# Optimization experiments

Measured on AMD Instinct MI355X. Metric: run time of the kernel, lower is better.

## Reference

```python
import jax, jax.numpy as jnp
import numpy as np

DV = 512   # node feature size
DE = 256   # edge feature size
N = 128    # valid node num (human_nums + obj_nums)
B = 8
K = 3      # propagate_layers
C = 117    # hoi_classes


def gru_cell(x, h, w_ih, w_hh, b_ih, b_hh):
    # PyTorch nn.GRU single step, gate order (r, z, n)
    gi = w_ih @ x + b_ih
    gh = w_hh @ h + b_hh
    ir, iz, inn = jnp.split(gi, 3)
    hr, hz, hn = jnp.split(gh, 3)
    r = jax.nn.sigmoid(ir + hr)
    z = jax.nn.sigmoid(iz + hz)
    n = jnp.tanh(inn + r * hn)
    return (1.0 - z) * n + z * h


def _run_graph(h, e, w_link, b_link, w_msg, b_msg, w_ih, w_hh, b_ih, b_hh):
    # h: [dv, N], e: [de, N, N]
    wl_j = w_link[:DV]          # applied to Feature[:dv, i, :] = h (column index j)
    wl_i = w_link[DV:2 * DV]    # applied to Feature[dv:2dv, :, i] = h (row index i)
    wl_e = w_link[2 * DV:]
    adj = jnp.zeros((N, N), h.dtype)
    for _ in range(K):
        # link function on Feature built under torch.no_grad -> stop_gradient
        hs = jax.lax.stop_gradient(h)
        es = jax.lax.stop_gradient(e)
        logits = (wl_i @ hs)[:, None] + (wl_j @ hs)[None, :] \
                 + jnp.einsum('c,cij->ij', wl_e, es) + b_link
        adj = jax.nn.sigmoid(logits)  # [N, N]

        def node_step(carry, i):
            h, e = carry
            h_v = h[:, i]                      # [dv]
            e_row = e[:, i, :]                 # [de, N] (rows < i already updated this round)
            comb = jnp.concatenate(
                [jnp.broadcast_to(h_v[:, None], (DV, N)), h, e_row], axis=0)  # [2dv+de, N]
            m = jax.nn.relu(w_msg @ comb + b_msg[:, None])                    # [de, N]
            e = e.at[:, i, :].set(m)
            m_sum = (m * adj[i][None, :]).sum(axis=1)                         # [de]
            h_new = gru_cell(m_sum, h_v, w_ih, w_hh, b_ih, b_hh)
            h = h.at[:, i].set(h_new)
            return (h, e), None

        (h, e), _ = jax.lax.scan(node_step, (h, e), jnp.arange(N))
    return adj, h


def setup_inputs() -> dict:
    key = jax.random.key(0)
    ks = jax.random.split(key, 8)
    s = 0.02
    return {
        "edge_features": jax.random.normal(ks[0], (B, N, N, DE), jnp.float32),
        "node_features": jax.random.normal(ks[1], (B, N, DV), jnp.float32),
        "adj_mat": jnp.zeros((B, N, N), jnp.float32),
        "node_labels": jnp.zeros((B, N, C), jnp.float32),
        "human_nums": jnp.full((B,), 32, jnp.int32),
        "obj_nums": jnp.full((B,), 96, jnp.int32),
        "w_link": jax.random.normal(ks[2], (2 * DV + DE,), jnp.float32) * s,
        "b_link": jnp.zeros((), jnp.float32),
        "w_msg": jax.random.normal(ks[3], (DE, 2 * DV + DE), jnp.float32) * s,
        "b_msg": jnp.zeros((DE,), jnp.float32),
        "w_ih": jax.random.normal(ks[4], (3 * DV, DE), jnp.float32) * s,
        "w_hh": jax.random.normal(ks[5], (3 * DV, DV), jnp.float32) * s,
        "b_ih": jnp.zeros((3 * DV,), jnp.float32),
        "b_hh": jnp.zeros((3 * DV,), jnp.float32),
        "w_ro": jax.random.normal(ks[6], (C, DV), jnp.float32) * s,
        "b_ro": jnp.zeros((C,), jnp.float32),
    }


def reference(edge_features, node_features, adj_mat, node_labels, human_nums,
              obj_nums, w_link, b_link, w_msg, b_msg, w_ih, w_hh, b_ih, b_hh,
              w_ro, b_ro):
    e0 = jnp.transpose(edge_features, (0, 3, 1, 2))  # [B, de, N, N]
    h0 = jnp.transpose(node_features, (0, 2, 1))     # [B, dv, N]
    run = jax.vmap(_run_graph, in_axes=(0, 0) + (None,) * 8)
    pred_adj_mat, h = run(h0, e0, w_link, b_link, w_msg, b_msg,
                          w_ih, w_hh, b_ih, b_hh)
    # readout on the final (post-last-update) node states
    pred_node_labels = jnp.einsum('cd,bdn->bnc', w_ro, h) + b_ro
    return pred_adj_mat, pred_node_labels
```

## Files before the change

### kernel.cpp

```cpp
#include <hip/hip_runtime.h>
#include <math.h>


#define NB 8
#define NN 128
#define DVV 512
#define DEE 256
#define NCC 117
#define SB 16
#define PGOFF 196608

typedef __attribute__((ext_vector_type(8))) short short8;
typedef __attribute__((ext_vector_type(4))) float f32x4;

__device__ __forceinline__ float sigmf(float x) {
  x = fminf(fmaxf(x, -30.f), 30.f);
  return 1.0f / (1.0f + __expf(-x));
}
__device__ __forceinline__ float tanhf_fast(float x) {
  x = fminf(fmaxf(x, -15.f), 15.f);
  float e = __expf(2.0f * x);
  return (e - 1.0f) / (e + 1.0f);
}
__device__ __forceinline__ unsigned short f2bf(float f) {
  union { float f; unsigned u; } v; v.f = f;
  unsigned u = v.u + 0x7FFFu + ((v.u >> 16) & 1u);
  return (unsigned short)(u >> 16);
}
__device__ __forceinline__ float bfu(unsigned short u) {
  union { unsigned u; float f; } v; v.u = ((unsigned)u) << 16; return v.f;
}

__global__ __launch_bounds__(256) void k_copy(const float* __restrict__ src, float* __restrict__ dst,
                                              unsigned short* __restrict__ hb) {
  int i = blockIdx.x * 256 + threadIdx.x;
  float4 v = ((const float4*)src)[i];
  ((float4*)dst)[i] = v;
  unsigned long long pk = (unsigned long long)f2bf(v.x) | ((unsigned long long)f2bf(v.y) << 16)
                        | ((unsigned long long)f2bf(v.z) << 32) | ((unsigned long long)f2bf(v.w) << 48);
  *(unsigned long long*)&hb[i * 4] = pk;
}

__global__ __launch_bounds__(256) void k_cvtw(const float* __restrict__ w_msg,
                                              unsigned short* __restrict__ w3b) {
  int idx = blockIdx.x * 256 + threadIdx.x;
  int r = idx >> 8, c = idx & 255;
  w3b[idx] = f2bf(w_msg[(size_t)r * 1280 + 1024 + c]);
}

__global__ __launch_bounds__(128) void k_av(const float* __restrict__ h, const float* __restrict__ w_link,
                                            float* __restrict__ av) {
  int b = blockIdx.x >> 7, n = blockIdx.x & 127;
  int lane = threadIdx.x & 63, half = threadIdx.x >> 6;
  const float* hc = h + (size_t)((b << 7) + n) * DVV;
  const float* w = w_link + half * DVV;
  float acc = 0.f;
#pragma unroll
  for (int t = 0; t < 8; ++t) { int d = lane + (t << 6); acc += w[d] * hc[d]; }
#pragma unroll
  for (int off = 32; off; off >>= 1) acc += __shfl_down(acc, off);
  if (lane == 0) av[(b << 8) + half * NN + n] = acc;
}

template <int FIRST>
__global__ __launch_bounds__(256) void k_plogit_mfma(
    const float* edge, const unsigned short* eP16in, const unsigned short* __restrict__ w3b,
    const float* __restrict__ w_link, const float* __restrict__ av,
    const float* __restrict__ b_link, unsigned short* eP16out, float* __restrict__ adj_out) {
  int b = blockIdx.x >> 7, i = blockIdx.x & 127;
  __shared__ unsigned short eL[128 * 264];
  int tid = threadIdx.x;

  if (FIRST) {
    const float* s0 = edge + (size_t)(b * NN + i) * NN * DEE;
    for (int l = tid; l < 4096; l += 256) {
      int j = l >> 5, c0 = (l & 31) * 8;
      float4 v0 = *(const float4*)&s0[(size_t)j * DEE + c0];
      float4 v1 = *(const float4*)&s0[(size_t)j * DEE + c0 + 4];
      unsigned long long p0 = (unsigned long long)f2bf(v0.x) | ((unsigned long long)f2bf(v0.y) << 16)
                            | ((unsigned long long)f2bf(v0.z) << 32) | ((unsigned long long)f2bf(v0.w) << 48);
      unsigned long long p1 = (unsigned long long)f2bf(v1.x) | ((unsigned long long)f2bf(v1.y) << 16)
                            | ((unsigned long long)f2bf(v1.z) << 32) | ((unsigned long long)f2bf(v1.w) << 48);
      *(unsigned long long*)&eL[j * 264 + c0] = p0;
      *(unsigned long long*)&eL[j * 264 + c0 + 4] = p1;
    }
  } else {
    const unsigned short* s0 = eP16in + (size_t)(b * NN + i) * DEE * NN;
#pragma unroll
    for (int t = 0; t < 2; ++t) {
      int blk = tid + t * 256;
      int c0 = (blk >> 4) * 8, j0 = (blk & 15) * 8;
      short8 rows[8];
#pragma unroll
      for (int cc = 0; cc < 8; ++cc)
        rows[cc] = *(const short8*)&s0[(size_t)(c0 + cc) * NN + j0];
#pragma unroll
      for (int jj = 0; jj < 8; ++jj) {
        short8 o;
#pragma unroll
        for (int cc = 0; cc < 8; ++cc) o[cc] = rows[cc][jj];
        *(short8*)&eL[(j0 + jj) * 264 + c0] = o;
      }
    }
  }
  __syncthreads();

  float accLE = 0.f;
  if (tid < NN) {
    const unsigned short* row = &eL[tid * 264];
    for (int c = 0; c < DEE; ++c) accLE += w_link[1024 + c] * bfu(row[c]);
  }

  const int w = tid >> 6, l = tid & 63;
  const int lm = l & 15, lg = l >> 4;
  f32x4 acc[4][8];
#pragma unroll
  for (int a = 0; a < 4; ++a)
#pragma unroll
    for (int jt = 0; jt < 8; ++jt) acc[a][jt] = (f32x4){0.f, 0.f, 0.f, 0.f};

#pragma unroll
  for (int kk = 0; kk < 8; ++kk) {
    short8 afr[4];
#pragma unroll
    for (int a = 0; a < 4; ++a)
      afr[a] = *(const short8*)&w3b[(size_t)(64 * w + 16 * a + lm) * 256 + 32 * kk + 8 * lg];
#pragma unroll
    for (int jt = 0; jt < 8; ++jt) {
      short8 bfr = *(const short8*)&eL[(16 * jt + lm) * 264 + 32 * kk + 8 * lg];
#pragma unroll
      for (int a = 0; a < 4; ++a)
        acc[a][jt] = __builtin_amdgcn_mfma_f32_16x16x32_bf16(afr[a], bfr, acc[a][jt], 0, 0, 0);
    }
  }

  unsigned short* Pout = eP16out + (size_t)(b * NN + i) * DEE * NN;
#pragma unroll
  for (int a = 0; a < 4; ++a) {
    int rbase = 64 * w + 16 * a + 4 * lg;
#pragma unroll
    for (int jt = 0; jt < 8; ++jt) {
      int j = 16 * jt + lm;
#pragma unroll
      for (int q = 0; q < 4; ++q)
        Pout[(size_t)(rbase + q) * NN + j] = f2bf(acc[a][jt][q]);
    }
  }
  if (tid < NN) {
    float x = av[(b << 8) + NN + i] + av[(b << 8) + tid] + accLE + b_link[0];
    adj_out[((size_t)b * NN + i) * NN + tid] = sigmf(x);
  }
}

__global__ __launch_bounds__(256) void k_wh3(const float* __restrict__ w_hh, const float* __restrict__ w_msg,
                                             const float* __restrict__ b_hh, const float* __restrict__ b_msg,
                                             const float* __restrict__ h, float* __restrict__ GHo,
                                             float* __restrict__ Uo, float* __restrict__ Go) {
  int bx = blockIdx.x, b = blockIdx.y;
  const float* W; const float* bias; float* out; int ldw, R, r0;
  if (bx < 96)       { W = w_hh;        ldw = 512;  R = 1536; bias = b_hh;   out = GHo; r0 = bx * 16; }
  else if (bx < 112) { W = w_msg;       ldw = 1280; R = 256;  bias = b_msg;  out = Uo;  r0 = (bx - 96) * 16; }
  else               { W = w_msg + 512; ldw = 1280; R = 256;  bias = nullptr; out = Go; r0 = (bx - 112) * 16; }
  __shared__ float hT[128][129];
  __shared__ float wT[16][129];
  __shared__ float outT[16][129];
  int tid = threadIdx.x;
  int n = tid & 127, rr = tid >> 7;
  float acc8[8] = {0, 0, 0, 0, 0, 0, 0, 0};
  for (int dc = 0; dc < DVV; dc += 128) {
    if (dc) __syncthreads();
    for (int l = tid * 4; l < 16384; l += 1024) {
      int nn = l >> 7, d = l & 127;
      float4 v = *(const float4*)&h[((size_t)(b << 7) + nn) * DVV + dc + d];
      hT[d + 0][nn] = v.x; hT[d + 1][nn] = v.y; hT[d + 2][nn] = v.z; hT[d + 3][nn] = v.w;
    }
    for (int l = tid; l < 2048; l += 256) {
      int r = l >> 7, d = l & 127;
      wT[r][d] = W[(size_t)(r0 + r) * ldw + dc + d];
    }
    __syncthreads();
    for (int d = 0; d < 128; ++d) {
      float hval = hT[d][n];
#pragma unroll
      for (int r8 = 0; r8 < 8; ++r8) acc8[r8] += wT[rr * 8 + r8][d] * hval;
    }
  }
#pragma unroll
  for (int r8 = 0; r8 < 8; ++r8) {
    int r = rr * 8 + r8;
    outT[r][n] = acc8[r8] + (bias ? bias[r0 + r] : 0.0f);
  }
  __syncthreads();
  int n2 = tid >> 1, q = tid & 1;
  size_t base = ((size_t)(b << 7) + n2) * R + r0 + q * 8;
  float4 o0; o0.x = outT[q * 8 + 0][n2]; o0.y = outT[q * 8 + 1][n2]; o0.z = outT[q * 8 + 2][n2]; o0.w = outT[q * 8 + 3][n2];
  float4 o1; o1.x = outT[q * 8 + 4][n2]; o1.y = outT[q * 8 + 5][n2]; o1.z = outT[q * 8 + 6][n2]; o1.w = outT[q * 8 + 7][n2];
  *(float4*)&out[base] = o0;
  *(float4*)&out[base + 4] = o1;
}

template <int WRITE_E>
__global__ __launch_bounds__(256) void k_scan10(
    unsigned short* eP16, const float* __restrict__ adj, const float* __restrict__ GH,
    const float* __restrict__ U, const float* __restrict__ Gini, float* __restrict__ h,
    unsigned short* __restrict__ hb, const float* __restrict__ w_ih,
    const float* __restrict__ b_ih, const float* __restrict__ w_msg,
    float* __restrict__ pg, unsigned* __restrict__ flags, int kround) {
  const int s = blockIdx.x, b = blockIdx.y, tid = threadIdx.x;
  __shared__ float wihL[16 * 1540];
  __shared__ __align__(16) float w2L[16 * 520];
  __shared__ __align__(16) float GL[16 * 132];
  __shared__ float hnL[DVV];
  __shared__ float msL[16];

  for (int l = tid; l < 1536 * 16; l += 256) {
    int r = l >> 4, c = l & 15;
    wihL[c * 1540 + r] = w_ih[(size_t)r * 256 + 16 * s + c];
  }
  for (int l = tid; l < 16 * 128; l += 256) {
    int c = l >> 7, d4 = (l & 127) * 4;
    *(float4*)&w2L[c * 520 + d4] = *(const float4*)&w_msg[(size_t)(16 * s + c) * 1280 + 512 + d4];
  }
  for (int l = tid; l < 2048; l += 256) {
    int c = l & 15, j = l >> 4;
    GL[c * 132 + j] = Gini[((size_t)b * NN + j) * DEE + 16 * s + c];
  }
  float bi0 = b_ih[tid], bi1 = b_ih[tid + 256];
  float bi2 = b_ih[512 + tid], bi3 = b_ih[768 + tid];
  float bi4 = b_ih[1024 + tid], bi5 = b_ih[1280 + tid];

  const int c_loc = tid >> 4, jg = tid & 15, j0 = jg << 3;

  short8 Pv; float4 A0, A1; float uu;
  float hv0, hv1, ghr0, ghr1, ghz0, ghz1, ghn0, ghn1;
  {
    size_t rE = ((size_t)(b * NN + 0) * DEE + 16 * s + c_loc) * NN + j0;
    Pv = *(const short8*)&eP16[rE];
    size_t rA = (size_t)(b * NN + 0) * NN + j0;
    A0 = *(const float4*)&adj[rA]; A1 = *(const float4*)&adj[rA + 4];
    uu = U[(size_t)(b * NN + 0) * DEE + 16 * s + c_loc];
    size_t rH = (size_t)(b * NN + 0) * DVV;
    hv0 = h[rH + tid]; hv1 = h[rH + tid + 256];
    size_t rG = (size_t)(b * NN + 0) * 1536;
    ghr0 = GH[rG + tid]; ghr1 = GH[rG + tid + 256];
    ghz0 = GH[rG + 512 + tid]; ghz1 = GH[rG + 768 + tid];
    ghn0 = GH[rG + 1024 + tid]; ghn1 = GH[rG + 1280 + tid];
  }

  for (int i = 0; i < NN; ++i) {
    float* pgb = pg + (size_t)(i & 1) * PGOFF + (size_t)((b << 4) + s) * 1536;
    float* pgr = pg + (size_t)(i & 1) * PGOFF + (size_t)(b << 4) * 1536;
    __syncthreads();

    float acc;
    {
      const float* gl = &GL[c_loc * 132 + j0];
      float4 g0 = *(const float4*)&gl[0];
      float4 g1 = *(const float4*)&gl[4];
      float m0 = fmaxf(uu + g0.x + bfu((unsigned short)Pv[0]), 0.f);
      float m1 = fmaxf(uu + g0.y + bfu((unsigned short)Pv[1]), 0.f);
      float m2 = fmaxf(uu + g0.z + bfu((unsigned short)Pv[2]), 0.f);
      float m3 = fmaxf(uu + g0.w + bfu((unsigned short)Pv[3]), 0.f);
      float m4 = fmaxf(uu + g1.x + bfu((unsigned short)Pv[4]), 0.f);
      float m5 = fmaxf(uu + g1.y + bfu((unsigned short)Pv[5]), 0.f);
      float m6 = fmaxf(uu + g1.z + bfu((unsigned short)Pv[6]), 0.f);
      float m7 = fmaxf(uu + g1.w + bfu((unsigned short)Pv[7]), 0.f);
      acc = A0.x * m0 + A0.y * m1 + A0.z * m2 + A0.w * m3
          + A1.x * m4 + A1.y * m5 + A1.z * m6 + A1.w * m7;
      if (WRITE_E) {
        size_t rE = ((size_t)(b * NN + i) * DEE + 16 * s + c_loc) * NN + j0;
        short8 mw;
        mw[0] = (short)f2bf(m0); mw[1] = (short)f2bf(m1); mw[2] = (short)f2bf(m2); mw[3] = (short)f2bf(m3);
        mw[4] = (short)f2bf(m4); mw[5] = (short)f2bf(m5); mw[6] = (short)f2bf(m6); mw[7] = (short)f2bf(m7);
        *(short8*)&eP16[rE] = mw;
      }
    }
    {
      int in = (i < NN - 1) ? i + 1 : NN - 1;
      size_t rE = ((size_t)(b * NN + in) * DEE + 16 * s + c_loc) * NN + j0;
      Pv = *(const short8*)&eP16[rE];
      size_t rA = (size_t)(b * NN + in) * NN + j0;
      A0 = *(const float4*)&adj[rA]; A1 = *(const float4*)&adj[rA + 4];
      uu = U[(size_t)(b * NN + in) * DEE + 16 * s + c_loc];
    }
    acc += __shfl_down(acc, 8);
    acc += __shfl_down(acc, 4);
    acc += __shfl_down(acc, 2);
    acc += __shfl_down(acc, 1);
    if (jg == 0) msL[c_loc] = acc;
    __syncthreads();

    {
      float ms[16];
#pragma unroll
      for (int c = 0; c < 16; ++c) ms[c] = msL[c];
#pragma unroll
      for (int u = 0; u < 6; ++u) {
        int r = tid + (u << 8);
        float pa = 0.f;
#pragma unroll
        for (int c = 0; c < 16; ++c) pa += wihL[c * 1540 + r] * ms[c];
        __hip_atomic_store(&pgb[r], pa, __ATOMIC_RELAXED, __HIP_MEMORY_SCOPE_SYSTEM);
      }
    }

    {
      unsigned tgt = (unsigned)(kround * NN + i + 1);
      __syncthreads();
      if (tid < 64) {
        if (tid == 0)
          __hip_atomic_store(&flags[(((b << 4) + s) << 5)], tgt, __ATOMIC_RELAXED,
                             __HIP_MEMORY_SCOPE_SYSTEM);
        unsigned* fp = &flags[(((b << 4) + (tid & 15)) << 5)];
        for (;;) {
          unsigned v = __hip_atomic_load(fp, __ATOMIC_RELAXED, __HIP_MEMORY_SCOPE_SYSTEM);
          if (!__any(v < tgt)) break;
          __builtin_amdgcn_s_sleep(1);
        }
      }
      __syncthreads();
    }

    {
      float sr0 = bi0, sr1 = bi1, sz0 = bi2, sz1 = bi3, sn0 = bi4, sn1 = bi5;
#pragma unroll
      for (int ss = 0; ss < 16; ++ss) {
        float* p = pgr + (size_t)ss * 1536;
        sr0 += __hip_atomic_load(&p[tid],        __ATOMIC_RELAXED, __HIP_MEMORY_SCOPE_SYSTEM);
        sr1 += __hip_atomic_load(&p[tid + 256],  __ATOMIC_RELAXED, __HIP_MEMORY_SCOPE_SYSTEM);
        sz0 += __hip_atomic_load(&p[512 + tid],  __ATOMIC_RELAXED, __HIP_MEMORY_SCOPE_SYSTEM);
        sz1 += __hip_atomic_load(&p[768 + tid],  __ATOMIC_RELAXED, __HIP_MEMORY_SCOPE_SYSTEM);
        sn0 += __hip_atomic_load(&p[1024 + tid], __ATOMIC_RELAXED, __HIP_MEMORY_SCOPE_SYSTEM);
        sn1 += __hip_atomic_load(&p[1280 + tid], __ATOMIC_RELAXED, __HIP_MEMORY_SCOPE_SYSTEM);
      }
      float rg0 = sigmf(sr0 + ghr0), rg1 = sigmf(sr1 + ghr1);
      float z0 = sigmf(sz0 + ghz0),  z1 = sigmf(sz1 + ghz1);
      float nv0 = tanhf_fast(sn0 + rg0 * ghn0);
      float nv1 = tanhf_fast(sn1 + rg1 * ghn1);
      float hn0 = (1.f - z0) * nv0 + z0 * hv0;
      float hn1 = (1.f - z1) * nv1 + z1 * hv1;
      hnL[tid] = hn0; hnL[tid + 256] = hn1;
      size_t rH = (size_t)(b * NN + i) * DVV;
      if ((tid >> 5) == s)         { h[rH + tid] = hn0;       hb[rH + tid] = f2bf(hn0); }
      if (((tid + 256) >> 5) == s) { h[rH + tid + 256] = hn1; hb[rH + tid + 256] = f2bf(hn1); }
    }
    {
      int in = (i < NN - 1) ? i + 1 : NN - 1;
      size_t rH = (size_t)(b * NN + in) * DVV;
      hv0 = h[rH + tid]; hv1 = h[rH + tid + 256];
      size_t rG = (size_t)(b * NN + in) * 1536;
      ghr0 = GH[rG + tid]; ghr1 = GH[rG + tid + 256];
      ghz0 = GH[rG + 512 + tid]; ghz1 = GH[rG + 768 + tid];
      ghn0 = GH[rG + 1024 + tid]; ghn1 = GH[rG + 1280 + tid];
    }
    __syncthreads();

    {
      int cw = tid >> 4, dg = tid & 15;
      float acc2 = 0.f;
#pragma unroll
      for (int it = 0; it < 32; ++it) {
        int d = dg + (it << 4);
        acc2 += w2L[cw * 520 + d] * hnL[d];
      }
      acc2 += __shfl_down(acc2, 8);
      acc2 += __shfl_down(acc2, 4);
      acc2 += __shfl_down(acc2, 2);
      acc2 += __shfl_down(acc2, 1);
      if (dg == 0) GL[cw * 132 + i] = acc2;
    }
  }
}

__global__ __launch_bounds__(128) void k_labels(const float* __restrict__ h, const float* __restrict__ w_ro,
                                                const float* __restrict__ b_ro, float* __restrict__ out) {
  int b = blockIdx.x >> 7, n = blockIdx.x & 127;
  __shared__ __align__(16) float hr[512];
  int tid = threadIdx.x;
  *(float4*)&hr[tid * 4] = *(const float4*)&h[(size_t)((b << 7) + n) * DVV + tid * 4];
  __syncthreads();
  if (tid < NCC) {
    const float* w = w_ro + (size_t)tid * DVV;
    float acc = b_ro[tid];
    for (int d = 0; d < DVV; d += 4) {
      float4 wv = *(const float4*)&w[d];
      acc += wv.x * hr[d] + wv.y * hr[d + 1] + wv.z * hr[d + 2] + wv.w * hr[d + 3];
    }
    out[(size_t)((b << 7) + n) * NCC + tid] = acc;
  }
}

extern "C" void kernel_launch(void* const* d_in, const int* in_sizes, int n_in,
                              void* d_out, int out_size, void* d_ws, size_t ws_size,
                              hipStream_t stream) {
  const float* edge   = (const float*)d_in[0];
  const float* node   = (const float*)d_in[1];
  const float* w_link = (const float*)d_in[6];
  const float* b_link = (const float*)d_in[7];
  const float* w_msg  = (const float*)d_in[8];
  const float* b_msg  = (const float*)d_in[9];
  const float* w_ih   = (const float*)d_in[10];
  const float* w_hh   = (const float*)d_in[11];
  const float* b_ih   = (const float*)d_in[12];
  const float* b_hh   = (const float*)d_in[13];
  const float* w_ro   = (const float*)d_in[14];
  const float* b_ro   = (const float*)d_in[15];
  float* out = (float*)d_out;
  float* ws  = (float*)d_ws;

  unsigned short* eP16 = (unsigned short*)ws;
  unsigned short* hb   = (unsigned short*)(ws + 21000000);
  float* h_buf  = ws + 33554432ull;
  float* GH_buf = h_buf + 524288;
  float* U_buf  = GH_buf + 1572864;
  float* G_buf  = U_buf + 262144;
  float* lE_buf = G_buf + 262144;
  float* av_buf = lE_buf + 131072;
  float* pg_buf = av_buf + 2048;
  unsigned* flags = (unsigned*)(pg_buf + 2 * PGOFF);
  unsigned short* w3b = (unsigned short*)lE_buf;
  size_t need_bytes = 36710304ull * 4ull;
  if (ws_size < need_bytes) return;

  hipMemsetAsync(flags, 0, 4096 * sizeof(unsigned), stream);
  k_copy<<<512, 256, 0, stream>>>(node, h_buf, hb);
  k_cvtw<<<256, 256, 0, stream>>>(w_msg, w3b);

  for (int k = 0; k < 3; ++k) {
    k_av<<<1024, 128, 0, stream>>>(h_buf, w_link, av_buf);
    if (k == 0) k_plogit_mfma<1><<<1024, 256, 0, stream>>>(edge, eP16, w3b, w_link, av_buf, b_link, eP16, out);
    else        k_plogit_mfma<0><<<1024, 256, 0, stream>>>(edge, eP16, w3b, w_link, av_buf, b_link, eP16, out);
    k_wh3<<<dim3(128, 8), 256, 0, stream>>>(w_hh, w_msg, b_hh, b_msg, h_buf, GH_buf, U_buf, G_buf);
    if (k < 2) k_scan10<1><<<dim3(SB, NB), 256, 0, stream>>>(eP16, out, GH_buf, U_buf, G_buf, h_buf, hb,
                                                             w_ih, b_ih, w_msg, pg_buf, flags, k);
    else       k_scan10<0><<<dim3(SB, NB), 256, 0, stream>>>(eP16, out, GH_buf, U_buf, G_buf, h_buf, hb,
                                                             w_ih, b_ih, w_msg, pg_buf, flags, k);
  }
  k_labels<<<1024, 128, 0, stream>>>(h_buf, w_ro, b_ro, out + 131072);
}
```

Before: 2.310 ms.

## Reduce cross-block GRU input partials with float atomics in triple-buffered slots

Replaces the per-block partial-sum buffers, where each of the 16 blocks stored its partial and every block then read all 16 partials, with atomic float adds into one shared slot per batch. Three rotating slots are used, and each block zeroes its share of the next slot ahead of time, so each step's reduction reads 6 values per thread instead of 96. The goal is to cut cross-block memory traffic on the serial critical path of the scan. In exchange it relies on atomic add throughput and contention, and it makes the summation order nondeterministic.

```diff
diff --git a/kernel.cpp b/kernel.cpp
--- a/kernel.cpp
+++ b/kernel.cpp
@@ -8,7 +8,7 @@
 #define DEE 256
 #define NCC 117
 #define SB 16
-#define PGOFF 196608
+#define GISLOT 12288
 
 typedef __attribute__((ext_vector_type(8))) short short8;
 typedef __attribute__((ext_vector_type(4))) float f32x4;
@@ -200,12 +200,12 @@
 }
 
 template <int WRITE_E>
-__global__ __launch_bounds__(256) void k_scan10(
+__global__ __launch_bounds__(256) void k_scan13(
     unsigned short* eP16, const float* __restrict__ adj, const float* __restrict__ GH,
     const float* __restrict__ U, const float* __restrict__ Gini, float* __restrict__ h,
     unsigned short* __restrict__ hb, const float* __restrict__ w_ih,
     const float* __restrict__ b_ih, const float* __restrict__ w_msg,
-    float* __restrict__ pg, unsigned* __restrict__ flags, int kround) {
+    float* __restrict__ gi, unsigned* __restrict__ flags, int kround) {
   const int s = blockIdx.x, b = blockIdx.y, tid = threadIdx.x;
   __shared__ float wihL[16 * 1540];
   __shared__ __align__(16) float w2L[16 * 520];
@@ -248,8 +248,9 @@
   }
 
   for (int i = 0; i < NN; ++i) {
-    float* pgb = pg + (size_t)(i & 1) * PGOFF + (size_t)((b << 4) + s) * 1536;
-    float* pgr = pg + (size_t)(i & 1) * PGOFF + (size_t)(b << 4) * 1536;
+    int g = kround * NN + i;
+    float* giA = gi + (size_t)(g % 3) * GISLOT + (size_t)b * 1536;
+    float* giZ = gi + (size_t)((g + 1) % 3) * GISLOT + (size_t)b * 1536;
     __syncthreads();
 
     float acc;
@@ -300,12 +301,14 @@
         float pa = 0.f;
 #pragma unroll
         for (int c = 0; c < 16; ++c) pa += wihL[c * 1540 + r] * ms[c];
-        __hip_atomic_store(&pgb[r], pa, __ATOMIC_RELAXED, __HIP_MEMORY_SCOPE_SYSTEM);
+        (void)__hip_atomic_fetch_add(&giA[r], pa, __ATOMIC_RELAXED, __HIP_MEMORY_SCOPE_SYSTEM);
       }
-    }
-
-    {
-      unsigned tgt = (unsigned)(kround * NN + i + 1);
+      if (tid < 96)
+        __hip_atomic_store(&giZ[96 * s + tid], 0.f, __ATOMIC_RELAXED, __HIP_MEMORY_SCOPE_SYSTEM);
+    }
+
+    {
+      unsigned tgt = (unsigned)(g + 1);
       __syncthreads();
       if (tid < 64) {
         if (tid == 0)
@@ -322,17 +325,12 @@
     }
 
     {
-      float sr0 = bi0, sr1 = bi1, sz0 = bi2, sz1 = bi3, sn0 = bi4, sn1 = bi5;
-#pragma unroll
-      for (int ss = 0; ss < 16; ++ss) {
-        float* p = pgr + (size_t)ss * 1536;
-        sr0 += __hip_atomic_load(&p[tid],        __ATOMIC_RELAXED, __HIP_MEMORY_SCOPE_SYSTEM);
-        sr1 += __hip_atomic_load(&p[tid + 256],  __ATOMIC_RELAXED, __HIP_MEMORY_SCOPE_SYSTEM);
-        sz0 += __hip_atomic_load(&p[512 + tid],  __ATOMIC_RELAXED, __HIP_MEMORY_SCOPE_SYSTEM);
-        sz1 += __hip_atomic_load(&p[768 + tid],  __ATOMIC_RELAXED, __HIP_MEMORY_SCOPE_SYSTEM);
-        sn0 += __hip_atomic_load(&p[1024 + tid], __ATOMIC_RELAXED, __HIP_MEMORY_SCOPE_SYSTEM);
-        sn1 += __hip_atomic_load(&p[1280 + tid], __ATOMIC_RELAXED, __HIP_MEMORY_SCOPE_SYSTEM);
-      }
+      float sr0 = bi0 + __hip_atomic_load(&giA[tid],        __ATOMIC_RELAXED, __HIP_MEMORY_SCOPE_SYSTEM);
+      float sr1 = bi1 + __hip_atomic_load(&giA[tid + 256],  __ATOMIC_RELAXED, __HIP_MEMORY_SCOPE_SYSTEM);
+      float sz0 = bi2 + __hip_atomic_load(&giA[512 + tid],  __ATOMIC_RELAXED, __HIP_MEMORY_SCOPE_SYSTEM);
+      float sz1 = bi3 + __hip_atomic_load(&giA[768 + tid],  __ATOMIC_RELAXED, __HIP_MEMORY_SCOPE_SYSTEM);
+      float sn0 = bi4 + __hip_atomic_load(&giA[1024 + tid], __ATOMIC_RELAXED, __HIP_MEMORY_SCOPE_SYSTEM);
+      float sn1 = bi5 + __hip_atomic_load(&giA[1280 + tid], __ATOMIC_RELAXED, __HIP_MEMORY_SCOPE_SYSTEM);
       float rg0 = sigmf(sr0 + ghr0), rg1 = sigmf(sr1 + ghr1);
       float z0 = sigmf(sz0 + ghz0),  z1 = sigmf(sz1 + ghz1);
       float nv0 = tanhf_fast(sn0 + rg0 * ghn0);
@@ -416,13 +414,13 @@
   float* G_buf  = U_buf + 262144;
   float* lE_buf = G_buf + 262144;
   float* av_buf = lE_buf + 131072;
-  float* pg_buf = av_buf + 2048;
-  unsigned* flags = (unsigned*)(pg_buf + 2 * PGOFF);
+  float* gi_buf = av_buf + 2048;
+  unsigned* flags = (unsigned*)(gi_buf + 3 * GISLOT);
   unsigned short* w3b = (unsigned short*)lE_buf;
   size_t need_bytes = 36710304ull * 4ull;
   if (ws_size < need_bytes) return;
 
-  hipMemsetAsync(flags, 0, 4096 * sizeof(unsigned), stream);
+  hipMemsetAsync(gi_buf, 0, (3 * GISLOT + 4096) * sizeof(float), stream);
   k_copy<<<512, 256, 0, stream>>>(node, h_buf, hb);
   k_cvtw<<<256, 256, 0, stream>>>(w_msg, w3b);
 
@@ -431,10 +429,10 @@
     if (k == 0) k_plogit_mfma<1><<<1024, 256, 0, stream>>>(edge, eP16, w3b, w_link, av_buf, b_link, eP16, out);
     else        k_plogit_mfma<0><<<1024, 256, 0, stream>>>(edge, eP16, w3b, w_link, av_buf, b_link, eP16, out);
     k_wh3<<<dim3(128, 8), 256, 0, stream>>>(w_hh, w_msg, b_hh, b_msg, h_buf, GH_buf, U_buf, G_buf);
-    if (k < 2) k_scan10<1><<<dim3(SB, NB), 256, 0, stream>>>(eP16, out, GH_buf, U_buf, G_buf, h_buf, hb,
-                                                             w_ih, b_ih, w_msg, pg_buf, flags, k);
-    else       k_scan10<0><<<dim3(SB, NB), 256, 0, stream>>>(eP16, out, GH_buf, U_buf, G_buf, h_buf, hb,
-                                                             w_ih, b_ih, w_msg, pg_buf, flags, k);
+    if (k < 2) k_scan13<1><<<dim3(SB, NB), 256, 0, stream>>>(eP16, out, GH_buf, U_buf, G_buf, h_buf, hb,
+                                                             w_ih, b_ih, w_msg, gi_buf, flags, k);
+    else       k_scan13<0><<<dim3(SB, NB), 256, 0, stream>>>(eP16, out, GH_buf, U_buf, G_buf, h_buf, hb,
+                                                             w_ih, b_ih, w_msg, gi_buf, flags, k);
   }
   k_labels<<<1024, 128, 0, stream>>>(h_buf, w_ro, b_ro, out + 131072);
 }
```

Result: faster. 1.953 ms (-15.5%).
